# Kernel tuning notes

Measured on AMD Instinct MI355X. Metric: run time of the kernel, lower is better.

Reference implementation:

```python
import jax, jax.numpy as jnp
import numpy as np

B, H, W, C = 8, 128, 128, 256
WS, SS, NH = 8, 4, 8          # window size, shift size, num heads
HD = C // NH                   # head dim = 32
N = WS * WS                    # tokens per window = 64
NW = (H // WS) * (W // WS)     # windows per image = 256


def _rel_pos_index():
    coords = np.stack(np.meshgrid(np.arange(WS), np.arange(WS), indexing='ij'))  # (2,WS,WS)
    cf = coords.reshape(2, -1)
    rc = (cf[:, :, None] - cf[:, None, :]).transpose(1, 2, 0)
    rc[:, :, 0] += WS - 1
    rc[:, :, 1] += WS - 1
    rc[:, :, 0] *= 2 * WS - 1
    return rc.sum(-1)  # (N, N) int


def _attn_mask():
    # shift mask for SW-MSA, built from static shapes (matches torch img_mask construction)
    img = np.zeros((1, H, W, 1))
    sl = (slice(0, -WS), slice(-WS, -SS), slice(-SS, None))
    cnt = 0
    for h in sl:
        for w in sl:
            img[:, h, w, :] = cnt
            cnt += 1
    mw = img.reshape(1, H // WS, WS, W // WS, WS, 1).transpose(0, 1, 3, 2, 4, 5).reshape(-1, N)
    am = mw[:, None, :] - mw[:, :, None]  # (NW, N, N)
    return np.where(am != 0, -100.0, 0.0).astype(np.float32)


RPI = jnp.asarray(_rel_pos_index())      # (N, N)
AMASK = jnp.asarray(_attn_mask())        # (NW, N, N)


def _ln(x, g, b):
    m = x.mean(-1, keepdims=True)
    v = x.var(-1, keepdims=True)
    return (x - m) / jnp.sqrt(v + 1e-5) * g + b


def setup_inputs() -> dict:
    key = jax.random.key(0)
    ks = jax.random.split(key, 8)
    s = lambda k, shp, sc: jax.random.normal(k, shp, jnp.float32) * sc
    return {
        'x': s(ks[0], (B, H * W, C), 1.0),
        'norm1_g': jnp.ones((C,), jnp.float32), 'norm1_b': jnp.zeros((C,), jnp.float32),
        'qkv_w': s(ks[1], (3 * C, C), 0.02), 'qkv_b': jnp.zeros((3 * C,), jnp.float32),
        'rpb_table': s(ks[2], ((2 * WS - 1) ** 2, NH), 0.02),
        'proj_w': s(ks[3], (C, C), 0.02), 'proj_b': jnp.zeros((C,), jnp.float32),
        'norm2_g': jnp.ones((C,), jnp.float32), 'norm2_b': jnp.zeros((C,), jnp.float32),
        'fc1_w': s(ks[4], (4 * C, C), 0.02), 'fc1_b': jnp.zeros((4 * C,), jnp.float32),
        'fc2_w': s(ks[5], (C, 4 * C), 0.02), 'fc2_b': jnp.zeros((C,), jnp.float32),
    }


def reference(x, norm1_g, norm1_b, qkv_w, qkv_b, rpb_table, proj_w, proj_b,
              norm2_g, norm2_b, fc1_w, fc1_b, fc2_w, fc2_b):
    shortcut = x
    h = _ln(x, norm1_g, norm1_b).reshape(B, H, W, C)
    # cyclic shift
    h = jnp.roll(h, (-SS, -SS), axis=(1, 2))
    # window partition -> (B*NW, N, C)
    xw = h.reshape(B, H // WS, WS, W // WS, WS, C).transpose(0, 1, 3, 2, 4, 5).reshape(-1, N, C)
    qkv = (xw @ qkv_w.T + qkv_b).reshape(-1, N, 3, NH, HD).transpose(2, 0, 3, 1, 4)
    q, k, v = qkv[0], qkv[1], qkv[2]           # (B*NW, NH, N, HD)
    attn = jnp.einsum('bhnd,bhmd->bhnm', q * (float(HD) ** -0.5), k)
    bias = rpb_table[RPI.reshape(-1)].reshape(N, N, NH).transpose(2, 0, 1)  # (NH, N, N)
    attn = attn + bias[None]
    attn = attn.reshape(B, NW, NH, N, N) + AMASK[None, :, None]
    attn = jax.nn.softmax(attn.reshape(-1, NH, N, N), axis=-1)
    xw = jnp.einsum('bhnm,bhmd->bnhd', attn, v).reshape(-1, N, C)
    xw = xw @ proj_w.T + proj_b
    # window reverse + reverse shift
    h = xw.reshape(B, H // WS, W // WS, WS, WS, C).transpose(0, 1, 3, 2, 4, 5).reshape(B, H, W, C)
    h = jnp.roll(h, (SS, SS), axis=(1, 2)).reshape(B, H * W, C)
    x = shortcut + h
    # MLP block
    m = _ln(x, norm2_g, norm2_b)
    m = jax.nn.gelu(m @ fc1_w.T + fc1_b, approximate=False) @ fc2_w.T + fc2_b
    return x + m
```

## Files before the change

kernel.cpp:

```cpp
#include <hip/hip_runtime.h>
#include <hip/hip_bf16.h>
#include <math.h>

#define B_   8
#define H_   128
#define W_   128
#define C_   256
#define WS_  8
#define SS_  4
#define NH_  8
#define HD_  32
#define MROWS 131072

typedef short bf16x8 __attribute__((ext_vector_type(8)));
typedef float f32x4  __attribute__((ext_vector_type(4)));

__device__ __forceinline__ unsigned short f2bf(float f) {
    unsigned int u = __float_as_uint(f);
    u += 0x7fffu + ((u >> 16) & 1u);
    return (unsigned short)(u >> 16);
}

__device__ __forceinline__ unsigned int pk2(float a, float b) {
    __hip_bfloat162 h = __float22bfloat162_rn(make_float2(a, b));
    unsigned int u;
    __builtin_memcpy(&u, &h, 4);
    return u;
}

__device__ __forceinline__ void gload16(const unsigned short* g, unsigned short* l) {
    __builtin_amdgcn_global_load_lds(
        (const __attribute__((address_space(1))) unsigned int*)(const void*)g,
        (__attribute__((address_space(3))) unsigned int*)(void*)l, 16, 0, 0);
}

__device__ __forceinline__ float fast_gelu2(float v) {
    return v * __builtin_amdgcn_rcpf(1.0f + __expf(-1.702f * v));
}

__global__ __launch_bounds__(256) void cvt4(const float* __restrict__ s,
                                            unsigned short* __restrict__ d, int n) {
    const int i = (blockIdx.x * 256 + threadIdx.x) * 4;
    if (i >= n) return;
    const float4 v = *(const float4*)(s + i);
    ushort4 o;
    o.x = f2bf(v.x); o.y = f2bf(v.y); o.z = f2bf(v.z); o.w = f2bf(v.w);
    *(ushort4*)(d + i) = o;
}

template<int SHIFT>
__global__ __launch_bounds__(256) void ln_kernel(const float* __restrict__ in,
                                                 const float* __restrict__ g,
                                                 const float* __restrict__ b,
                                                 unsigned short* __restrict__ out) {
    const int wid  = threadIdx.x >> 6;
    const int lane = threadIdx.x & 63;
    const int row  = blockIdx.x * 4 + wid;

    int src;
    if (SHIFT) {
        const int bimg = row >> 14;
        const int rem  = row & 16383;
        const int win  = rem >> 6;
        const int tok  = rem & 63;
        const int hp = (win >> 4) * 8 + (tok >> 3);
        const int wp = (win & 15) * 8 + (tok & 7);
        const int ho = (hp + SS_) & (H_ - 1);
        const int wo = (wp + SS_) & (W_ - 1);
        src = (bimg << 14) + ho * W_ + wo;
    } else {
        src = row;
    }

    const float4 v = ((const float4*)(in + (size_t)src * C_))[lane];
    float s  = v.x + v.y + v.z + v.w;
    float ss = v.x*v.x + v.y*v.y + v.z*v.z + v.w*v.w;
#pragma unroll
    for (int o = 1; o < 64; o <<= 1) {
        s  += __shfl_xor(s,  o, 64);
        ss += __shfl_xor(ss, o, 64);
    }
    const float mean = s * (1.0f / C_);
    const float var  = ss * (1.0f / C_) - mean * mean;
    const float rstd = rsqrtf(var + 1e-5f);

    const float4 gg = ((const float4*)g)[lane];
    const float4 bb = ((const float4*)b)[lane];
    ushort4 o4;
    o4.x = f2bf((v.x - mean) * rstd * gg.x + bb.x);
    o4.y = f2bf((v.y - mean) * rstd * gg.y + bb.y);
    o4.z = f2bf((v.z - mean) * rstd * gg.z + bb.z);
    o4.w = f2bf((v.w - mean) * rstd * gg.w + bb.w);
    *(ushort4*)(out + (size_t)row * C_ + lane * 4) = o4;
}

template<int N>
__global__ __launch_bounds__(256, 2) void gemm_nloop(const unsigned short* __restrict__ A,
                                                     const unsigned short* __restrict__ W,
                                                     const float* __restrict__ bias,
                                                     unsigned short* __restrict__ Cout) {
    __shared__ unsigned short W_lds[2][64 * 256];

    const int t    = threadIdx.x;
    const int wave = t >> 6, lane = t & 63;
    const int fr   = lane & 15, h = lane >> 4;
    const int m0   = blockIdx.x * 128;
    constexpr int NT = N / 64;

    bf16x8 aw[2][8];
    const unsigned short* Abase = A + (size_t)(m0 + wave * 32 + fr) * 256 + h * 8;
#pragma unroll
    for (int mi = 0; mi < 2; ++mi)
#pragma unroll
        for (int ks = 0; ks < 8; ++ks)
            aw[mi][ks] = *(const bf16x8*)(Abase + mi * 16 * 256 + ks * 32);

    auto stage = [&](int b, int nt) {
        const unsigned short* Wt = W + (size_t)nt * 64 * 256;
#pragma unroll
        for (int q = 0; q < 8; ++q) {
            const int d    = q * 4096 + t * 16;
            const int row  = d >> 9;
            const int colb = (d & 511) ^ ((row & 7) << 4);
            gload16(Wt + (size_t)row * 256 + (colb >> 1),
                    &W_lds[b][(q * 4096 + wave * 1024) >> 1]);
        }
    };

    stage(0, 0);
    __syncthreads();

    for (int nt = 0; nt < NT; ++nt) {
        if (nt + 1 < NT) stage((nt + 1) & 1, nt + 1);

        const char* buf = (const char*)W_lds[nt & 1];
        f32x4 acc[2][4] = {};
#pragma unroll
        for (int nj = 0; nj < 4; ++nj) {
            const int   wrow = nj * 16 + fr;
            const char* wb   = buf + wrow * 512;
            const int   swz  = (fr & 7) << 4;
            bf16x8 wf[8];
#pragma unroll
            for (int ks = 0; ks < 8; ++ks)
                wf[ks] = *(const bf16x8*)(wb + ((ks * 64 + h * 16) ^ swz));
#pragma unroll
            for (int ks = 0; ks < 8; ++ks) {
                acc[0][nj] = __builtin_amdgcn_mfma_f32_16x16x32_bf16(wf[ks], aw[0][ks], acc[0][nj], 0, 0, 0);
                acc[1][nj] = __builtin_amdgcn_mfma_f32_16x16x32_bf16(wf[ks], aw[1][ks], acc[1][nj], 0, 0, 0);
            }
        }

#pragma unroll
        for (int nj = 0; nj < 4; ++nj) {
            const int n = nt * 64 + nj * 16 + h * 4;
            const float4 bb = *(const float4*)&bias[n];
#pragma unroll
            for (int mi = 0; mi < 2; ++mi) {
                const int m = m0 + wave * 32 + mi * 16 + fr;
                uint2 pk;
                pk.x = pk2(acc[mi][nj][0] + bb.x, acc[mi][nj][1] + bb.y);
                pk.y = pk2(acc[mi][nj][2] + bb.z, acc[mi][nj][3] + bb.w);
                *(uint2*)&Cout[(size_t)m * N + n] = pk;
            }
        }
        __syncthreads();
    }
}

__global__ __launch_bounds__(512, 2) void mlp_fused(const unsigned short* __restrict__ A,
                                                    const unsigned short* __restrict__ W1,
                                                    const float* __restrict__ b1,
                                                    const unsigned short* __restrict__ W2,
                                                    const float* __restrict__ b2,
                                                    float* __restrict__ out) {
    __shared__ unsigned short W1_lds[2][64 * 256];
    __shared__ unsigned short W2_lds[256 * 64];
    __shared__ unsigned short G_lds[256 * 64];

    const int t    = threadIdx.x;
    const int wave = t >> 6, lane = t & 63;
    const int fr   = lane & 15, h = lane >> 4;
    const int wr   = wave >> 2, wc = wave & 3;
    const int m0   = blockIdx.x * 256;
    const int swz  = (fr & 7) << 4;

    bf16x8 aw[2][8];
    const unsigned short* Abase = A + (size_t)(m0 + wave * 32 + fr) * 256 + h * 8;
#pragma unroll
    for (int mi = 0; mi < 2; ++mi)
#pragma unroll
        for (int ks = 0; ks < 8; ++ks)
            aw[mi][ks] = *(const bf16x8*)(Abase + mi * 16 * 256 + ks * 32);

    auto stageW1 = [&](int b, int c) {
        const unsigned short* Wt = W1 + (size_t)c * 64 * 256;
#pragma unroll
        for (int q = 0; q < 4; ++q) {
            const int d    = q * 8192 + t * 16;
            const int row  = d >> 9;
            const int colb = (d & 511) ^ ((row & 7) << 4);
            gload16(Wt + (size_t)row * 256 + (colb >> 1),
                    &W1_lds[b][(q * 8192 + wave * 1024) >> 1]);
        }
    };
    auto stageW2 = [&](int c) {
#pragma unroll
        for (int q = 0; q < 4; ++q) {
            const int d    = q * 8192 + t * 16;
            const int row  = d >> 7;
            const int colb = (d & 127) ^ ((row & 7) << 4);
            gload16(W2 + (size_t)row * 1024 + c * 64 + (colb >> 1),
                    (unsigned short*)((char*)W2_lds + q * 8192 + wave * 1024));
        }
    };

    stageW1(0, 0);

    f32x4 acc2[8][4] = {};

    for (int c = 0; c < 16; ++c) {
        stageW2(c);
        if (c + 1 < 16) {
            stageW1((c + 1) & 1, c + 1);
            asm volatile("s_waitcnt vmcnt(8)" ::: "memory");
        } else {
            asm volatile("s_waitcnt vmcnt(4)" ::: "memory");
        }
        __builtin_amdgcn_sched_barrier(0);
        __builtin_amdgcn_s_barrier();

        const char* buf = (const char*)W1_lds[c & 1];
#pragma unroll
        for (int nj = 0; nj < 4; ++nj) {
            const int   wrow = nj * 16 + fr;
            const char* wb   = buf + wrow * 512;
            bf16x8 wf[8];
#pragma unroll
            for (int ks = 0; ks < 8; ++ks)
                wf[ks] = *(const bf16x8*)(wb + ((ks * 64 + h * 16) ^ swz));
            f32x4 g0 = {}, g1 = {};
#pragma unroll
            for (int ks = 0; ks < 8; ++ks) {
                g0 = __builtin_amdgcn_mfma_f32_16x16x32_bf16(wf[ks], aw[0][ks], g0, 0, 0, 0);
                g1 = __builtin_amdgcn_mfma_f32_16x16x32_bf16(wf[ks], aw[1][ks], g1, 0, 0, 0);
            }
            const float4 bb = *(const float4*)&b1[c * 64 + nj * 16 + h * 4];
            {
                const int row = wave * 32 + fr;
                const int off = (nj * 32 + h * 8) ^ ((row & 7) << 4);
                uint2 pk;
                pk.x = pk2(fast_gelu2(g0[0] + bb.x), fast_gelu2(g0[1] + bb.y));
                pk.y = pk2(fast_gelu2(g0[2] + bb.z), fast_gelu2(g0[3] + bb.w));
                *(uint2*)((char*)G_lds + row * 128 + off) = pk;
            }
            {
                const int row = wave * 32 + 16 + fr;
                const int off = (nj * 32 + h * 8) ^ ((row & 7) << 4);
                uint2 pk;
                pk.x = pk2(fast_gelu2(g1[0] + bb.x), fast_gelu2(g1[1] + bb.y));
                pk.y = pk2(fast_gelu2(g1[2] + bb.z), fast_gelu2(g1[3] + bb.w));
                *(uint2*)((char*)G_lds + row * 128 + off) = pk;
            }
        }

        if (c + 1 < 16)
            asm volatile("s_waitcnt vmcnt(4) lgkmcnt(0)" ::: "memory");
        else
            asm volatile("s_waitcnt vmcnt(0) lgkmcnt(0)" ::: "memory");
        __builtin_amdgcn_sched_barrier(0);
        __builtin_amdgcn_s_barrier();

#pragma unroll
        for (int ks = 0; ks < 2; ++ks) {
            bf16x8 gf[8];
#pragma unroll
            for (int mi2 = 0; mi2 < 8; ++mi2) {
                const int grow = wr * 128 + mi2 * 16 + fr;
                gf[mi2] = *(const bf16x8*)((char*)G_lds + grow * 128
                                           + ((ks * 64 + h * 16) ^ swz));
            }
#pragma unroll
            for (int nj2 = 0; nj2 < 4; ++nj2) {
                const int wrow2 = wc * 64 + nj2 * 16 + fr;
                const bf16x8 w2f = *(const bf16x8*)((char*)W2_lds + wrow2 * 128
                                                    + ((ks * 64 + h * 16) ^ swz));
#pragma unroll
                for (int mi2 = 0; mi2 < 8; ++mi2)
                    acc2[mi2][nj2] = __builtin_amdgcn_mfma_f32_16x16x32_bf16(
                        w2f, gf[mi2], acc2[mi2][nj2], 0, 0, 0);
            }
        }
        __builtin_amdgcn_s_barrier();
    }

    float4 bv[4];
#pragma unroll
    for (int nj2 = 0; nj2 < 4; ++nj2)
        bv[nj2] = *(const float4*)&b2[wc * 64 + nj2 * 16 + h * 4];

#pragma unroll
    for (int mi2 = 0; mi2 < 8; ++mi2) {
        const int m = m0 + wr * 128 + mi2 * 16 + fr;
#pragma unroll
        for (int nj2 = 0; nj2 < 4; ++nj2) {
            const int n = wc * 64 + nj2 * 16 + h * 4;
            const size_t idx = (size_t)m * 256 + n;
            const float4 r4 = *(const float4*)&out[idx];
            float4 o;
            o.x = acc2[mi2][nj2][0] + bv[nj2].x + r4.x;
            o.y = acc2[mi2][nj2][1] + bv[nj2].y + r4.y;
            o.z = acc2[mi2][nj2][2] + bv[nj2].z + r4.z;
            o.w = acc2[mi2][nj2][3] + bv[nj2].w + r4.w;
            *(float4*)&out[idx] = o;
        }
    }
}

__global__ __launch_bounds__(256, 2) void proj_ln2(const unsigned short* __restrict__ A,
                                                   const unsigned short* __restrict__ W,
                                                   const float* __restrict__ bias,
                                                   const float* __restrict__ resid,
                                                   const float* __restrict__ g2,
                                                   const float* __restrict__ b2,
                                                   float* __restrict__ out,
                                                   unsigned short* __restrict__ ln2out) {
    __shared__ unsigned short W_lds[2][64 * 256];

    const int t    = threadIdx.x;
    const int wave = t >> 6, lane = t & 63;
    const int fr   = lane & 15, h = lane >> 4;
    const int m0   = blockIdx.x * 128;

    bf16x8 aw[2][8];
    const unsigned short* Abase = A + (size_t)(m0 + wave * 32 + fr) * 256 + h * 8;
#pragma unroll
    for (int mi = 0; mi < 2; ++mi)
#pragma unroll
        for (int ks = 0; ks < 8; ++ks)
            aw[mi][ks] = *(const bf16x8*)(Abase + mi * 16 * 256 + ks * 32);

    auto stage = [&](int b, int nt) {
        const unsigned short* Wt = W + (size_t)nt * 64 * 256;
#pragma unroll
        for (int q = 0; q < 8; ++q) {
            const int d    = q * 4096 + t * 16;
            const int row  = d >> 9;
            const int colb = (d & 511) ^ ((row & 7) << 4);
            gload16(Wt + (size_t)row * 256 + (colb >> 1),
                    &W_lds[b][(q * 4096 + wave * 1024) >> 1]);
        }
    };

    stage(0, 0);
    __syncthreads();

    f32x4 acc[2][16] = {};
    for (int nt = 0; nt < 4; ++nt) {
        if (nt < 3) stage((nt + 1) & 1, nt + 1);
        const char* buf = (const char*)W_lds[nt & 1];
#pragma unroll
        for (int nj = 0; nj < 4; ++nj) {
            const int   wrow = nj * 16 + fr;
            const char* wb   = buf + wrow * 512;
            const int   swz  = (fr & 7) << 4;
            bf16x8 wf[8];
#pragma unroll
            for (int ks = 0; ks < 8; ++ks)
                wf[ks] = *(const bf16x8*)(wb + ((ks * 64 + h * 16) ^ swz));
            switch (nt) {
            case 0:
#pragma unroll
                for (int ks = 0; ks < 8; ++ks) {
                    acc[0][0 + nj] = __builtin_amdgcn_mfma_f32_16x16x32_bf16(wf[ks], aw[0][ks], acc[0][0 + nj], 0, 0, 0);
                    acc[1][0 + nj] = __builtin_amdgcn_mfma_f32_16x16x32_bf16(wf[ks], aw[1][ks], acc[1][0 + nj], 0, 0, 0);
                } break;
            case 1:
#pragma unroll
                for (int ks = 0; ks < 8; ++ks) {
                    acc[0][4 + nj] = __builtin_amdgcn_mfma_f32_16x16x32_bf16(wf[ks], aw[0][ks], acc[0][4 + nj], 0, 0, 0);
                    acc[1][4 + nj] = __builtin_amdgcn_mfma_f32_16x16x32_bf16(wf[ks], aw[1][ks], acc[1][4 + nj], 0, 0, 0);
                } break;
            case 2:
#pragma unroll
                for (int ks = 0; ks < 8; ++ks) {
                    acc[0][8 + nj] = __builtin_amdgcn_mfma_f32_16x16x32_bf16(wf[ks], aw[0][ks], acc[0][8 + nj], 0, 0, 0);
                    acc[1][8 + nj] = __builtin_amdgcn_mfma_f32_16x16x32_bf16(wf[ks], aw[1][ks], acc[1][8 + nj], 0, 0, 0);
                } break;
            default:
#pragma unroll
                for (int ks = 0; ks < 8; ++ks) {
                    acc[0][12 + nj] = __builtin_amdgcn_mfma_f32_16x16x32_bf16(wf[ks], aw[0][ks], acc[0][12 + nj], 0, 0, 0);
                    acc[1][12 + nj] = __builtin_amdgcn_mfma_f32_16x16x32_bf16(wf[ks], aw[1][ks], acc[1][12 + nj], 0, 0, 0);
                } break;
            }
        }
        __syncthreads();
    }

#pragma unroll
    for (int mi = 0; mi < 2; ++mi) {
        const int m    = m0 + wave * 32 + mi * 16 + fr;
        const int bimg = m >> 14;
        const int rem  = m & 16383;
        const int win  = rem >> 6;
        const int tok  = rem & 63;
        const int hp = (win >> 4) * 8 + (tok >> 3);
        const int wp = (win & 15) * 8 + (tok & 7);
        const int ho = (hp + SS_) & (H_ - 1);
        const int wo = (wp + SS_) & (W_ - 1);
        const size_t drow = ((size_t)(bimg << 14) + ho * W_ + wo) * 256;

        float sum = 0.0f, ssum = 0.0f;
#pragma unroll
        for (int u = 0; u < 16; ++u) {
            const int n = (u >> 2) * 64 + (u & 3) * 16 + h * 4;
            const float4 bb = *(const float4*)&bias[n];
            const float4 r4 = *(const float4*)&resid[drow + n];
            float4 v;
            v.x = acc[mi][u][0] + bb.x + r4.x;
            v.y = acc[mi][u][1] + bb.y + r4.y;
            v.z = acc[mi][u][2] + bb.z + r4.z;
            v.w = acc[mi][u][3] + bb.w + r4.w;
            *(float4*)&out[drow + n] = v;
            sum  += v.x + v.y + v.z + v.w;
            ssum += v.x*v.x + v.y*v.y + v.z*v.z + v.w*v.w;
        }
        sum  += __shfl_xor(sum, 16, 64);  sum  += __shfl_xor(sum, 32, 64);
        ssum += __shfl_xor(ssum, 16, 64); ssum += __shfl_xor(ssum, 32, 64);
        const float mean = sum * (1.0f / 256.0f);
        const float rstd = rsqrtf(ssum * (1.0f / 256.0f) - mean * mean + 1e-5f);

#pragma unroll
        for (int u = 0; u < 16; ++u) {
            const int n = (u >> 2) * 64 + (u & 3) * 16 + h * 4;
            const float4 v  = *(const float4*)&out[drow + n];
            const float4 gg = *(const float4*)&g2[n];
            const float4 bb = *(const float4*)&b2[n];
            uint2 pk;
            pk.x = pk2((v.x - mean) * rstd * gg.x + bb.x,
                       (v.y - mean) * rstd * gg.y + bb.y);
            pk.y = pk2((v.z - mean) * rstd * gg.z + bb.z,
                       (v.w - mean) * rstd * gg.w + bb.w);
            *(uint2*)&ln2out[drow + n] = pk;
        }
    }
}

__device__ __forceinline__ int grp_(int p) { return p < (H_ - WS_) ? 0 : (p < (H_ - SS_) ? 1 : 2); }

__global__ __launch_bounds__(256) void attn_kernel(const unsigned short* __restrict__ qkv,
                                                   const float* __restrict__ rpb,
                                                   unsigned short* __restrict__ out) {
    __shared__ unsigned short P [4][64 * 72];
    __shared__ unsigned short Vt[4][32 * 72];
    __shared__ float rpb_s[232];

    const int t    = threadIdx.x;
    const int wid  = t >> 6, lane = t & 63;
    const int head = blockIdx.x & 7;
    const int win  = (blockIdx.x >> 3) * 4 + wid;
    const int fr   = lane & 15, h = lane >> 4;

    if (t < 225) rpb_s[t] = rpb[t * 8 + head];
    __syncthreads();

    const size_t qbase = (size_t)win * 64 * 768 + head * HD_;

    bf16x8 ak[4], bq[4];
#pragma unroll
    for (int ki = 0; ki < 4; ++ki)
        ak[ki] = *(const bf16x8*)&qkv[qbase + (size_t)(ki * 16 + fr) * 768 + 256 + h * 8];
#pragma unroll
    for (int qj = 0; qj < 4; ++qj)
        bq[qj] = *(const bf16x8*)&qkv[qbase + (size_t)(qj * 16 + fr) * 768 + h * 8];

    {
        const unsigned short* vrow = &qkv[qbase + (size_t)lane * 768 + 512];
#pragma unroll
        for (int dv = 0; dv < 32; dv += 8) {
            bf16x8 v8 = *(const bf16x8*)&vrow[dv];
#pragma unroll
            for (int j = 0; j < 8; ++j)
                Vt[wid][(dv + j) * 72 + lane] = ((unsigned short*)&v8)[j];
        }
    }

    f32x4 st[4][4] = {};
#pragma unroll
    for (int ki = 0; ki < 4; ++ki)
#pragma unroll
        for (int qj = 0; qj < 4; ++qj)
            st[ki][qj] = __builtin_amdgcn_mfma_f32_16x16x32_bf16(ak[ki], bq[qj], st[ki][qj], 0, 0, 0);

    const int wim = win & 255;
    const int whb = (wim >> 4) * 8, wwb = (wim & 15) * 8;
    const float qscale = 0.17677669529663687f;

#pragma unroll
    for (int qj = 0; qj < 4; ++qj) {
        const int q  = qj * 16 + fr;
        const int yq = q >> 3, xq = q & 7;
        const int gq = grp_(whb + yq) * 3 + grp_(wwb + xq);
        float s[16];
#pragma unroll
        for (int ki = 0; ki < 4; ++ki)
#pragma unroll
            for (int r = 0; r < 4; ++r) {
                const int k  = ki * 16 + h * 4 + r;
                const int yk = k >> 3, xk = k & 7;
                const int gk = grp_(whb + yk) * 3 + grp_(wwb + xk);
                float v = fmaf(st[ki][qj][r], qscale,
                               rpb_s[(yq - yk + 7) * 15 + (xq - xk + 7)]);
                if (gk != gq) v -= 100.0f;
                s[ki * 4 + r] = v;
            }
        float m = s[0];
#pragma unroll
        for (int i = 1; i < 16; ++i) m = fmaxf(m, s[i]);
        m = fmaxf(m, __shfl_xor(m, 16, 64));
        m = fmaxf(m, __shfl_xor(m, 32, 64));
        float sum = 0.0f;
#pragma unroll
        for (int i = 0; i < 16; ++i) { s[i] = __expf(s[i] - m); sum += s[i]; }
        sum += __shfl_xor(sum, 16, 64);
        sum += __shfl_xor(sum, 32, 64);
        const float rinv = __builtin_amdgcn_rcpf(sum);
#pragma unroll
        for (int ki = 0; ki < 4; ++ki)
#pragma unroll
            for (int rp = 0; rp < 4; rp += 2) {
                const unsigned int lo = f2bf(s[ki * 4 + rp]     * rinv);
                const unsigned int hi = f2bf(s[ki * 4 + rp + 1] * rinv);
                *(unsigned int*)&P[wid][q * 72 + ki * 16 + h * 4 + rp] = lo | (hi << 16);
            }
    }

    f32x4 oacc[4][2] = {};
#pragma unroll
    for (int ks = 0; ks < 2; ++ks) {
        bf16x8 pa[4], vb[2];
#pragma unroll
        for (int qi = 0; qi < 4; ++qi)
            pa[qi] = *(const bf16x8*)&P[wid][(qi * 16 + fr) * 72 + ks * 32 + h * 8];
#pragma unroll
        for (int nj = 0; nj < 2; ++nj)
            vb[nj] = *(const bf16x8*)&Vt[wid][(nj * 16 + fr) * 72 + ks * 32 + h * 8];
#pragma unroll
        for (int qi = 0; qi < 4; ++qi)
#pragma unroll
            for (int nj = 0; nj < 2; ++nj)
                oacc[qi][nj] = __builtin_amdgcn_mfma_f32_16x16x32_bf16(pa[qi], vb[nj], oacc[qi][nj], 0, 0, 0);
    }

#pragma unroll
    for (int qi = 0; qi < 4; ++qi)
#pragma unroll
        for (int nj = 0; nj < 2; ++nj)
#pragma unroll
            for (int r = 0; r < 4; ++r) {
                const int q = qi * 16 + h * 4 + r;
                const int d = nj * 16 + fr;
                out[((size_t)win * 64 + q) * C_ + head * HD_ + d] = f2bf(oacc[qi][nj][r]);
            }
}

extern "C" void kernel_launch(void* const* d_in, const int* in_sizes, int n_in,
                              void* d_out, int out_size, void* d_ws, size_t ws_size,
                              hipStream_t stream) {
    const float* x      = (const float*)d_in[0];
    const float* n1g    = (const float*)d_in[1];
    const float* n1b    = (const float*)d_in[2];
    const float* qkv_w  = (const float*)d_in[3];
    const float* qkv_b  = (const float*)d_in[4];
    const float* rpb    = (const float*)d_in[5];
    const float* proj_w = (const float*)d_in[6];
    const float* proj_b = (const float*)d_in[7];
    const float* n2g    = (const float*)d_in[8];
    const float* n2b    = (const float*)d_in[9];
    const float* fc1_w  = (const float*)d_in[10];
    const float* fc1_b  = (const float*)d_in[11];
    const float* fc2_w  = (const float*)d_in[12];
    const float* fc2_b  = (const float*)d_in[13];
    float* out = (float*)d_out;

    unsigned short* wq  = (unsigned short*)d_ws;
    unsigned short* rA  = wq + (1u << 20);
    unsigned short* rB  = rA + 33554432u;
    unsigned short* rB2 = rB + 100663296u;

    unsigned short* qkv_wb  = wq;
    unsigned short* proj_wb = wq + 196608;
    unsigned short* fc1_wb  = wq + 262144;
    unsigned short* fc2_wb  = wq + 524288;

    cvt4<<<192, 256, 0, stream>>>(qkv_w,  qkv_wb,  196608);
    cvt4<<<64,  256, 0, stream>>>(proj_w, proj_wb, 65536);
    cvt4<<<256, 256, 0, stream>>>(fc1_w,  fc1_wb,  262144);
    cvt4<<<256, 256, 0, stream>>>(fc2_w,  fc2_wb,  262144);

    ln_kernel<1><<<MROWS / 4, 256, 0, stream>>>(x, n1g, n1b, rA);
    gemm_nloop<768><<<MROWS / 128, 256, 0, stream>>>(rA, qkv_wb, qkv_b, rB);
    attn_kernel<<<(2048 / 4) * NH_, 256, 0, stream>>>(rB, rpb, rB2);
    proj_ln2<<<MROWS / 128, 256, 0, stream>>>(rB2, proj_wb, proj_b, x, n2g, n2b, out, rA);
    mlp_fused<<<MROWS / 256, 512, 0, stream>>>(rA, fc1_wb, fc1_b, fc2_wb, fc2_b, out);
}
```

Measured before the change: 629.3 us.

## Software-pipeline fused MLP with 32-wide hidden chunks and double-buffered G/W2

Restructures the fused MLP kernel so hidden chunks are 32 wide instead of 64, with W1, W2 and the GELU intermediate all double-buffered in LDS. FC1 for chunk c+1 is computed after FC2 for chunk c, and the next weight loads are issued ahead, so each iteration needs one barrier instead of two. The goal is to overlap the FC1/GELU phase with FC2 MFMAs and global loads, at the cost of more barrier iterations (32 vs 16), narrower K per step, and launch bounds lowered to one block per CU, which may cut occupancy.

```diff
diff --git a/kernel.cpp b/kernel.cpp
--- a/kernel.cpp
+++ b/kernel.cpp
@@ -168,22 +168,22 @@
     }
 }
 
-__global__ __launch_bounds__(512, 2) void mlp_fused(const unsigned short* __restrict__ A,
+__global__ __launch_bounds__(512, 1) void mlp_fused(const unsigned short* __restrict__ A,
                                                     const unsigned short* __restrict__ W1,
                                                     const float* __restrict__ b1,
                                                     const unsigned short* __restrict__ W2,
                                                     const float* __restrict__ b2,
                                                     float* __restrict__ out) {
-    __shared__ unsigned short W1_lds[2][64 * 256];
-    __shared__ unsigned short W2_lds[256 * 64];
-    __shared__ unsigned short G_lds[256 * 64];
+    __shared__ unsigned short W1_lds[2][32 * 256];
+    __shared__ unsigned short W2_lds[2][256 * 32];
+    __shared__ unsigned short G_lds [2][256 * 32];
 
     const int t    = threadIdx.x;
     const int wave = t >> 6, lane = t & 63;
     const int fr   = lane & 15, h = lane >> 4;
     const int wr   = wave >> 2, wc = wave & 3;
     const int m0   = blockIdx.x * 256;
-    const int swz  = (fr & 7) << 4;
+    constexpr int NC = 32;
 
     bf16x8 aw[2][8];
     const unsigned short* Abase = A + (size_t)(m0 + wave * 32 + fr) * 256 + h * 8;
@@ -194,9 +194,9 @@
             aw[mi][ks] = *(const bf16x8*)(Abase + mi * 16 * 256 + ks * 32);
 
     auto stageW1 = [&](int b, int c) {
-        const unsigned short* Wt = W1 + (size_t)c * 64 * 256;
-#pragma unroll
-        for (int q = 0; q < 4; ++q) {
+        const unsigned short* Wt = W1 + (size_t)c * 32 * 256;
+#pragma unroll
+        for (int q = 0; q < 2; ++q) {
             const int d    = q * 8192 + t * 16;
             const int row  = d >> 9;
             const int colb = (d & 511) ^ ((row & 7) << 4);
@@ -204,35 +204,22 @@
                     &W1_lds[b][(q * 8192 + wave * 1024) >> 1]);
         }
     };
-    auto stageW2 = [&](int c) {
-#pragma unroll
-        for (int q = 0; q < 4; ++q) {
+    auto stageW2 = [&](int b, int c) {
+#pragma unroll
+        for (int q = 0; q < 2; ++q) {
             const int d    = q * 8192 + t * 16;
-            const int row  = d >> 7;
-            const int colb = (d & 127) ^ ((row & 7) << 4);
-            gload16(W2 + (size_t)row * 1024 + c * 64 + (colb >> 1),
-                    (unsigned short*)((char*)W2_lds + q * 8192 + wave * 1024));
+            const int row  = d >> 6;
+            const int colb = (d & 63) ^ ((row & 3) << 4);
+            gload16(W2 + (size_t)row * 1024 + c * 32 + (colb >> 1),
+                    &W2_lds[b][(q * 8192 + wave * 1024) >> 1]);
         }
     };
 
-    stageW1(0, 0);
-
-    f32x4 acc2[8][4] = {};
-
-    for (int c = 0; c < 16; ++c) {
-        stageW2(c);
-        if (c + 1 < 16) {
-            stageW1((c + 1) & 1, c + 1);
-            asm volatile("s_waitcnt vmcnt(8)" ::: "memory");
-        } else {
-            asm volatile("s_waitcnt vmcnt(4)" ::: "memory");
-        }
-        __builtin_amdgcn_sched_barrier(0);
-        __builtin_amdgcn_s_barrier();
-
-        const char* buf = (const char*)W1_lds[c & 1];
-#pragma unroll
-        for (int nj = 0; nj < 4; ++nj) {
+    auto fc1 = [&](int cc, int gb) {
+        const char* buf = (const char*)W1_lds[cc & 1];
+        const int   swz = (fr & 7) << 4;
+#pragma unroll
+        for (int nj = 0; nj < 2; ++nj) {
             const int   wrow = nj * 16 + fr;
             const char* wb   = buf + wrow * 512;
             bf16x8 wf[8];
@@ -245,53 +232,65 @@
                 g0 = __builtin_amdgcn_mfma_f32_16x16x32_bf16(wf[ks], aw[0][ks], g0, 0, 0, 0);
                 g1 = __builtin_amdgcn_mfma_f32_16x16x32_bf16(wf[ks], aw[1][ks], g1, 0, 0, 0);
             }
-            const float4 bb = *(const float4*)&b1[c * 64 + nj * 16 + h * 4];
+            const float4 bb = *(const float4*)&b1[cc * 32 + nj * 16 + h * 4];
             {
                 const int row = wave * 32 + fr;
-                const int off = (nj * 32 + h * 8) ^ ((row & 7) << 4);
+                const int off = (nj * 32 + h * 8) ^ ((row & 3) << 4);
                 uint2 pk;
                 pk.x = pk2(fast_gelu2(g0[0] + bb.x), fast_gelu2(g0[1] + bb.y));
                 pk.y = pk2(fast_gelu2(g0[2] + bb.z), fast_gelu2(g0[3] + bb.w));
-                *(uint2*)((char*)G_lds + row * 128 + off) = pk;
+                *(uint2*)((char*)G_lds[gb] + row * 64 + off) = pk;
             }
             {
                 const int row = wave * 32 + 16 + fr;
-                const int off = (nj * 32 + h * 8) ^ ((row & 7) << 4);
+                const int off = (nj * 32 + h * 8) ^ ((row & 3) << 4);
                 uint2 pk;
                 pk.x = pk2(fast_gelu2(g1[0] + bb.x), fast_gelu2(g1[1] + bb.y));
                 pk.y = pk2(fast_gelu2(g1[2] + bb.z), fast_gelu2(g1[3] + bb.w));
-                *(uint2*)((char*)G_lds + row * 128 + off) = pk;
-            }
-        }
-
-        if (c + 1 < 16)
-            asm volatile("s_waitcnt vmcnt(4) lgkmcnt(0)" ::: "memory");
-        else
-            asm volatile("s_waitcnt vmcnt(0) lgkmcnt(0)" ::: "memory");
+                *(uint2*)((char*)G_lds[gb] + row * 64 + off) = pk;
+            }
+        }
+    };
+
+    f32x4 acc2[8][4] = {};
+
+    stageW1(0, 0);
+    stageW2(0, 0);
+    asm volatile("s_waitcnt vmcnt(0)" ::: "memory");
+    __builtin_amdgcn_sched_barrier(0);
+    __builtin_amdgcn_s_barrier();
+    stageW1(1, 1);
+    fc1(0, 0);
+
+    for (int c = 0; c < NC; ++c) {
+        asm volatile("s_waitcnt vmcnt(0) lgkmcnt(0)" ::: "memory");
         __builtin_amdgcn_sched_barrier(0);
         __builtin_amdgcn_s_barrier();
 
-#pragma unroll
-        for (int ks = 0; ks < 2; ++ks) {
+        if (c + 2 < NC) stageW1(c & 1, c + 2);
+        if (c + 1 < NC) stageW2((c + 1) & 1, c + 1);
+
+        {
+            const char* Gb = (const char*)G_lds[c & 1];
+            const char* Wb = (const char*)W2_lds[c & 1];
             bf16x8 gf[8];
 #pragma unroll
             for (int mi2 = 0; mi2 < 8; ++mi2) {
                 const int grow = wr * 128 + mi2 * 16 + fr;
-                gf[mi2] = *(const bf16x8*)((char*)G_lds + grow * 128
-                                           + ((ks * 64 + h * 16) ^ swz));
+                gf[mi2] = *(const bf16x8*)(Gb + grow * 64 + ((h * 16) ^ ((grow & 3) << 4)));
             }
 #pragma unroll
             for (int nj2 = 0; nj2 < 4; ++nj2) {
                 const int wrow2 = wc * 64 + nj2 * 16 + fr;
-                const bf16x8 w2f = *(const bf16x8*)((char*)W2_lds + wrow2 * 128
-                                                    + ((ks * 64 + h * 16) ^ swz));
+                const bf16x8 w2f = *(const bf16x8*)(Wb + wrow2 * 64 + ((h * 16) ^ ((wrow2 & 3) << 4)));
 #pragma unroll
                 for (int mi2 = 0; mi2 < 8; ++mi2)
                     acc2[mi2][nj2] = __builtin_amdgcn_mfma_f32_16x16x32_bf16(
                         w2f, gf[mi2], acc2[mi2][nj2], 0, 0, 0);
             }
         }
-        __builtin_amdgcn_s_barrier();
+
+        if (c + 1 < NC) fc1(c + 1, (c + 1) & 1);
     }
 
     float4 bv[4];
```

After: 631.1 us. About the same (+0.3%).
